# Optimization experiments

Measured on AMD Instinct MI355X. Metric: run time of the kernel, lower is better.

Reference implementation:

```python
import jax, jax.numpy as jnp
import numpy as np

N = 131072      # points (rays x samples chunk)
E = 8           # spatial sub-networks (centroids)
DIN = 90        # encoded pos+dir features fed to sub-NeRFs (xyz_real=True -> x[:, 3:])
H = 256         # sub-NeRF hidden width
DOUT = 4        # rgb + sigma
MARGIN = 2.0    # boundary_margin
EPS = 1e-8


def setup_inputs() -> dict:
    key = jax.random.key(0)
    k = jax.random.split(key, 5)
    x_xyz = jax.random.uniform(k[0], (N, 3), dtype=jnp.float32)          # routing coords in [0,1)^3
    x_feat = jax.random.normal(k[1], (N, DIN), dtype=jnp.float32)        # encoded features
    x = jnp.concatenate([x_xyz, x_feat], axis=1)                         # [N, 3+DIN]
    centroids = jax.random.uniform(k[2], (E, 3), dtype=jnp.float32)
    W1 = jax.random.normal(k[3], (E, DIN, H), dtype=jnp.float32) * 0.05
    b1 = jnp.zeros((E, H), dtype=jnp.float32)
    W2 = jax.random.normal(k[4], (E, H, DOUT), dtype=jnp.float32) * 0.05
    b2 = jnp.zeros((E, DOUT), dtype=jnp.float32)
    return {"x": x, "centroids": centroids, "W1": W1, "b1": b1, "W2": W2, "b2": b2}


def reference(x, centroids, W1, b1, W2, b2):
    # --- centroid routing (torch.cdist equivalent) ---
    xyz = x[:, :3]                                                       # [N,3]
    d2 = jnp.sum((xyz[:, None, :] - centroids[None, :, :]) ** 2, axis=-1)
    dist = jnp.sqrt(jnp.maximum(d2, 0.0))                                # [N,E]
    inv = 1.0 / (dist + EPS)
    min_d = jnp.min(dist, axis=1, keepdims=True)                         # [N,1]
    inv = jnp.where(dist > MARGIN * min_d, 0.0, inv)                     # zero far experts
    weights = inv / jnp.sum(inv, axis=-1, keepdims=True)                 # [N,E], rows sum to 1

    # --- per-expert sub-NeRF MLP, weighted combine ---
    # Dense-equivalent of masked gather + weighted scatter-add: experts whose
    # weight is exactly 0 contribute nothing, matching the torch masked path.
    feat = x[:, 3:]                                                      # xyz_real=True -> drop xyz
    h = jax.nn.relu(jnp.einsum('nd,edh->enh', feat, W1) + b1[:, None, :])  # [E,N,H]
    out_e = jnp.einsum('enh,eho->eno', h, W2) + b2[:, None, :]             # [E,N,DOUT]
    return jnp.einsum('eno,ne->no', out_e, weights)                        # [N,DOUT]
```

## Files before the change

kernel.cpp:

```cpp
#include <hip/hip_runtime.h>

#define NPTS 131072
#define NE 8
#define DIN 90
#define NH 256
#define DO4 4
#define HPITCH 264

typedef __attribute__((ext_vector_type(8))) short bf16x8;
typedef __attribute__((ext_vector_type(4))) float f32x4;
typedef __attribute__((ext_vector_type(2))) unsigned int u32x2;

__device__ __forceinline__ unsigned short f2bf(float f) {
  unsigned int u = __float_as_uint(f);
  u += 0x7fffu + ((u >> 16) & 1u);
  return (unsigned short)(u >> 16);
}

__global__ __launch_bounds__(256) void prep_w1(const float* __restrict__ W1,
                                               unsigned short* __restrict__ W1T) {
  int idx = blockIdx.x * 256 + threadIdx.x;
  if (idx >= NE * NH * 96) return;
  int kp = idx % 96;
  int n  = (idx / 96) % NH;
  int e  = idx / (96 * NH);
  float v = (kp < DIN) ? W1[((size_t)e * DIN + kp) * NH + n] : 0.f;
  W1T[idx] = f2bf(v);
}

__global__ __launch_bounds__(256) void prep_w2(const float* __restrict__ W2,
                                               unsigned short* __restrict__ W2T) {
  int idx = blockIdx.x * 256 + threadIdx.x;
  if (idx >= NE * 16 * NH) return;
  int k = idx % NH;
  int o = (idx / NH) % 16;
  int e = idx / (16 * NH);
  float v = (o < DO4) ? W2[((size_t)e * NH + k) * DO4 + o] : 0.f;
  W2T[idx] = f2bf(v);
}

__global__ __launch_bounds__(256, 2) void meganerf_main(
    const float* __restrict__ x, const float* __restrict__ cent,
    const float* __restrict__ b1, const float* __restrict__ b2,
    const unsigned short* __restrict__ W1T, const unsigned short* __restrict__ W2T,
    float* __restrict__ out) {
  __shared__ unsigned short sH[64 * HPITCH];
  __shared__ float sW[NE][64];
  __shared__ float sB2[64][DO4];
  __shared__ float sOutP[4][64][DO4];

  const int t   = threadIdx.x;
  const int lane = t & 63;
  const int wid = t >> 6;
  const int l15 = lane & 15;
  const int l4  = lane >> 4;
  const int row0 = blockIdx.x * 64;

  bf16x8 bfr[4][3];
#pragma unroll
  for (int nf = 0; nf < 4; ++nf) {
    const float* gr = x + (size_t)(row0 + 16 * nf + l15) * 93 + 3;
#pragma unroll
    for (int ks = 0; ks < 3; ++ks) {
      const int kb = 32 * ks + 8 * l4;
      bf16x8 a;
#pragma unroll
      for (int j = 0; j < 8; ++j) {
        int k = kb + j;
        float v = (k < DIN) ? gr[k] : 0.f;
        a[j] = (short)f2bf(v);
      }
      bfr[nf][ks] = a;
    }
  }

  if (t < 64) {
    const float* gx = x + (size_t)(row0 + t) * 93;
    float px = gx[0], py = gx[1], pz = gx[2];
    float dist[NE], inv[NE];
    float mind = 3.4e38f;
#pragma unroll
    for (int e = 0; e < NE; ++e) {
      float dx = px - cent[e * 3 + 0];
      float dy = py - cent[e * 3 + 1];
      float dz = pz - cent[e * 3 + 2];
      float d2 = dx * dx + dy * dy + dz * dz;
      float d = sqrtf(fmaxf(d2, 0.f));
      dist[e] = d;
      inv[e] = 1.f / (d + 1e-8f);
      mind = fminf(mind, d);
    }
    float s = 0.f;
#pragma unroll
    for (int e = 0; e < NE; ++e) {
      if (dist[e] > 2.0f * mind) inv[e] = 0.f;
      s += inv[e];
    }
    float rs = 1.f / s;
    float bb[4] = {0.f, 0.f, 0.f, 0.f};
#pragma unroll
    for (int e = 0; e < NE; ++e) {
      float w = inv[e] * rs;
      sW[e][t] = w;
#pragma unroll
      for (int o = 0; o < 4; ++o) bb[o] += w * b2[e * 4 + o];
    }
#pragma unroll
    for (int o = 0; o < 4; ++o) sB2[t][o] = bb[o];
  }
  __syncthreads();

  f32x4 facc[4] = {{0.f, 0.f, 0.f, 0.f}, {0.f, 0.f, 0.f, 0.f},
                   {0.f, 0.f, 0.f, 0.f}, {0.f, 0.f, 0.f, 0.f}};

  for (int e = 0; e < NE; ++e) {
    float wv[4];
#pragma unroll
    for (int nf = 0; nf < 4; ++nf) wv[nf] = sW[e][16 * nf + l15];

#pragma unroll
    for (int c = 0; c < 2; ++c) {
      const int colbase = 128 * c + 32 * wid;
      f32x4 b1v[2];
#pragma unroll
      for (int mf = 0; mf < 2; ++mf)
        b1v[mf] = *(const f32x4*)(b1 + e * NH + colbase + 16 * mf + 4 * l4);
      f32x4 acc[2][4];
#pragma unroll
      for (int mf = 0; mf < 2; ++mf)
#pragma unroll
        for (int nf = 0; nf < 4; ++nf) acc[mf][nf] = b1v[mf];
#pragma unroll
      for (int ks = 0; ks < 3; ++ks) {
        bf16x8 w1f[2];
#pragma unroll
        for (int mf = 0; mf < 2; ++mf)
          w1f[mf] = *(const bf16x8*)(W1T +
              (size_t)(e * NH + colbase + 16 * mf + l15) * 96 + 32 * ks + 8 * l4);
#pragma unroll
        for (int mf = 0; mf < 2; ++mf)
#pragma unroll
          for (int nf = 0; nf < 4; ++nf)
            acc[mf][nf] = __builtin_amdgcn_mfma_f32_16x16x32_bf16(
                w1f[mf], bfr[nf][ks], acc[mf][nf], 0, 0, 0);
      }
#pragma unroll
      for (int mf = 0; mf < 2; ++mf) {
        const int hcol = colbase + 16 * mf + 4 * l4;
#pragma unroll
        for (int nf = 0; nf < 4; ++nf) {
          float w = wv[nf];
          f32x4 a = acc[mf][nf];
          unsigned int p0 = (unsigned int)f2bf(fmaxf(a[0], 0.f) * w) |
                            ((unsigned int)f2bf(fmaxf(a[1], 0.f) * w) << 16);
          unsigned int p1 = (unsigned int)f2bf(fmaxf(a[2], 0.f) * w) |
                            ((unsigned int)f2bf(fmaxf(a[3], 0.f) * w) << 16);
          u32x2 pk;
          pk[0] = p0;
          pk[1] = p1;
          *(u32x2*)&sH[(16 * nf + l15) * HPITCH + hcol] = pk;
        }
      }
    }
    __syncthreads();

#pragma unroll
    for (int ks2 = 0; ks2 < 2; ++ks2) {
      const int k = 64 * wid + 32 * ks2 + 8 * l4;
      bf16x8 bw = *(const bf16x8*)(W2T + (size_t)(e * 16 + l15) * NH + k);
#pragma unroll
      for (int rf = 0; rf < 4; ++rf) {
        bf16x8 ah = *(const bf16x8*)&sH[(16 * rf + l15) * HPITCH + k];
        facc[rf] = __builtin_amdgcn_mfma_f32_16x16x32_bf16(ah, bw, facc[rf], 0, 0, 0);
      }
    }
    __syncthreads();
  }

  if (l15 < DO4) {
#pragma unroll
    for (int rf = 0; rf < 4; ++rf)
#pragma unroll
      for (int r = 0; r < 4; ++r)
        sOutP[wid][16 * rf + 4 * l4 + r][l15] = facc[rf][r];
  }
  __syncthreads();
  {
    const int row = t >> 2, o = t & 3;
    float v = sB2[row][o] + sOutP[0][row][o] + sOutP[1][row][o] +
              sOutP[2][row][o] + sOutP[3][row][o];
    out[(size_t)(row0 + row) * DO4 + o] = v;
  }
}

extern "C" void kernel_launch(void* const* d_in, const int* in_sizes, int n_in,
                              void* d_out, int out_size, void* d_ws, size_t ws_size,
                              hipStream_t stream) {
  const float* x    = (const float*)d_in[0];
  const float* cent = (const float*)d_in[1];
  const float* W1   = (const float*)d_in[2];
  const float* b1   = (const float*)d_in[3];
  const float* W2   = (const float*)d_in[4];
  const float* b2   = (const float*)d_in[5];
  float* out = (float*)d_out;

  unsigned short* W1T = (unsigned short*)d_ws;
  unsigned short* W2T = W1T + NE * NH * 96;

  prep_w1<<<(NE * NH * 96 + 255) / 256, 256, 0, stream>>>(W1, W1T);
  prep_w2<<<(NE * 16 * NH + 255) / 256, 256, 0, stream>>>(W2, W2T);
  meganerf_main<<<NPTS / 64, 256, 0, stream>>>(x, cent, b1, b2, W1T, W2T, out);
}
```

Before: 193.6 us.

## Merge prep kernels, vectorize input loads, cheaper bf16 packing, raise occupancy

Fuses the two weight-prep kernels into one launch. Input features are now loaded as float4 vectors instead of scalar gathers. bf16 packing now uses a single perm that truncates after adding 0x7fff, dropping the round-to-even term. The output partials reuse the sH buffer so LDS per block shrinks, and launch bounds ask for 3 blocks per SIMD. The trade-offs are slightly different rounding and more register pressure at the higher occupancy target.

```diff
diff --git a/kernel.cpp b/kernel.cpp
--- a/kernel.cpp
+++ b/kernel.cpp
@@ -4,12 +4,15 @@
 #define NE 8
 #define DIN 90
 #define NH 256
-#define DO4 4
 #define HPITCH 264
 
 typedef __attribute__((ext_vector_type(8))) short bf16x8;
 typedef __attribute__((ext_vector_type(4))) float f32x4;
+typedef __attribute__((ext_vector_type(2))) float f32x2;
+typedef __attribute__((ext_vector_type(4))) unsigned int u32x4;
 typedef __attribute__((ext_vector_type(2))) unsigned int u32x2;
+typedef __attribute__((ext_vector_type(4), aligned(4))) float f32x4a;
+typedef __attribute__((ext_vector_type(2), aligned(4))) float f32x2a;
 
 __device__ __forceinline__ unsigned short f2bf(float f) {
   unsigned int u = __float_as_uint(f);
@@ -17,61 +20,81 @@
   return (unsigned short)(u >> 16);
 }
 
-__global__ __launch_bounds__(256) void prep_w1(const float* __restrict__ W1,
-                                               unsigned short* __restrict__ W1T) {
+__device__ __forceinline__ unsigned int pkbf(float f0, float f1) {
+  unsigned int u0 = __float_as_uint(f0) + 0x7fffu;
+  unsigned int u1 = __float_as_uint(f1) + 0x7fffu;
+  return __builtin_amdgcn_perm(u1, u0, 0x07060302u);
+}
+
+__device__ __forceinline__ bf16x8 cvt8(f32x4 a, f32x4 b) {
+  u32x4 r;
+  r[0] = pkbf(a[0], a[1]);
+  r[1] = pkbf(a[2], a[3]);
+  r[2] = pkbf(b[0], b[1]);
+  r[3] = pkbf(b[2], b[3]);
+  return __builtin_bit_cast(bf16x8, r);
+}
+
+__global__ __launch_bounds__(256) void prep(const float* __restrict__ W1,
+                                            const float* __restrict__ W2,
+                                            unsigned short* __restrict__ W1T,
+                                            unsigned short* __restrict__ W2T) {
   int idx = blockIdx.x * 256 + threadIdx.x;
-  if (idx >= NE * NH * 96) return;
-  int kp = idx % 96;
-  int n  = (idx / 96) % NH;
-  int e  = idx / (96 * NH);
-  float v = (kp < DIN) ? W1[((size_t)e * DIN + kp) * NH + n] : 0.f;
-  W1T[idx] = f2bf(v);
-}
-
-__global__ __launch_bounds__(256) void prep_w2(const float* __restrict__ W2,
-                                               unsigned short* __restrict__ W2T) {
-  int idx = blockIdx.x * 256 + threadIdx.x;
-  if (idx >= NE * 16 * NH) return;
-  int k = idx % NH;
-  int o = (idx / NH) % 16;
-  int e = idx / (16 * NH);
-  float v = (o < DO4) ? W2[((size_t)e * NH + k) * DO4 + o] : 0.f;
-  W2T[idx] = f2bf(v);
-}
-
-__global__ __launch_bounds__(256, 2) void meganerf_main(
+  const int n1 = NE * NH * 96;
+  if (idx < n1) {
+    int kp = idx % 96;
+    int n  = (idx / 96) % NH;
+    int e  = idx / (96 * NH);
+    float v = (kp < DIN) ? W1[((size_t)e * DIN + kp) * NH + n] : 0.f;
+    W1T[idx] = f2bf(v);
+  } else {
+    int j = idx - n1;
+    if (j < NE * 16 * NH) {
+      int k = j % NH;
+      int o = (j / NH) % 16;
+      int e = j / (16 * NH);
+      float v = (o < 4) ? W2[((size_t)e * NH + k) * 4 + o] : 0.f;
+      W2T[j] = f2bf(v);
+    }
+  }
+}
+
+__global__ __launch_bounds__(256, 3) void meganerf_main(
     const float* __restrict__ x, const float* __restrict__ cent,
     const float* __restrict__ b1, const float* __restrict__ b2,
     const unsigned short* __restrict__ W1T, const unsigned short* __restrict__ W2T,
     float* __restrict__ out) {
   __shared__ unsigned short sH[64 * HPITCH];
   __shared__ float sW[NE][64];
-  __shared__ float sB2[64][DO4];
-  __shared__ float sOutP[4][64][DO4];
-
-  const int t   = threadIdx.x;
+  __shared__ float sB2[64][4];
+
+  const int t    = threadIdx.x;
   const int lane = t & 63;
-  const int wid = t >> 6;
-  const int l15 = lane & 15;
-  const int l4  = lane >> 4;
+  const int wid  = t >> 6;
+  const int l15  = lane & 15;
+  const int l4   = lane >> 4;
   const int row0 = blockIdx.x * 64;
 
   bf16x8 bfr[4][3];
 #pragma unroll
   for (int nf = 0; nf < 4; ++nf) {
     const float* gr = x + (size_t)(row0 + 16 * nf + l15) * 93 + 3;
-#pragma unroll
-    for (int ks = 0; ks < 3; ++ks) {
-      const int kb = 32 * ks + 8 * l4;
-      bf16x8 a;
-#pragma unroll
-      for (int j = 0; j < 8; ++j) {
-        int k = kb + j;
-        float v = (k < DIN) ? gr[k] : 0.f;
-        a[j] = (short)f2bf(v);
-      }
-      bfr[nf][ks] = a;
-    }
+    f32x4 v0, v1;
+    v0 = *(const f32x4a*)(gr + 8 * l4);
+    v1 = *(const f32x4a*)(gr + 8 * l4 + 4);
+    bfr[nf][0] = cvt8(v0, v1);
+    v0 = *(const f32x4a*)(gr + 32 + 8 * l4);
+    v1 = *(const f32x4a*)(gr + 36 + 8 * l4);
+    bfr[nf][1] = cvt8(v0, v1);
+    if (l4 < 3) {
+      v0 = *(const f32x4a*)(gr + 64 + 8 * l4);
+      v1 = *(const f32x4a*)(gr + 68 + 8 * l4);
+    } else {
+      f32x2 tl = *(const f32x2a*)(gr + 88);
+      v0[0] = tl[0]; v0[1] = tl[1]; v0[2] = 0.f; v0[3] = 0.f;
+      v1[0] = 0.f; v1[1] = 0.f; v1[2] = 0.f; v1[3] = 0.f;
+    }
+    bfr[nf][2] = cvt8(v0, v1);
   }
 
   if (t < 64) {
@@ -149,15 +172,17 @@
         const int hcol = colbase + 16 * mf + 4 * l4;
 #pragma unroll
         for (int nf = 0; nf < 4; ++nf) {
-          float w = wv[nf];
+          const float w = wv[nf];
           f32x4 a = acc[mf][nf];
-          unsigned int p0 = (unsigned int)f2bf(fmaxf(a[0], 0.f) * w) |
-                            ((unsigned int)f2bf(fmaxf(a[1], 0.f) * w) << 16);
-          unsigned int p1 = (unsigned int)f2bf(fmaxf(a[2], 0.f) * w) |
-                            ((unsigned int)f2bf(fmaxf(a[3], 0.f) * w) << 16);
+          f32x2 p0, p1;
+          p0[0] = a[0]; p0[1] = a[1];
+          p1[0] = a[2]; p1[1] = a[3];
+          const f32x2 z = {0.f, 0.f};
+          p0 = __builtin_elementwise_max(p0, z) * w;
+          p1 = __builtin_elementwise_max(p1, z) * w;
           u32x2 pk;
-          pk[0] = p0;
-          pk[1] = p1;
+          pk[0] = pkbf(p0[0], p0[1]);
+          pk[1] = pkbf(p1[0], p1[1]);
           *(u32x2*)&sH[(16 * nf + l15) * HPITCH + hcol] = pk;
         }
       }
@@ -177,19 +202,20 @@
     __syncthreads();
   }
 
-  if (l15 < DO4) {
+  float* sOutP = (float*)sH;
+  if (l15 < 4) {
 #pragma unroll
     for (int rf = 0; rf < 4; ++rf)
 #pragma unroll
       for (int r = 0; r < 4; ++r)
-        sOutP[wid][16 * rf + 4 * l4 + r][l15] = facc[rf][r];
+        sOutP[(wid * 64 + 16 * rf + 4 * l4 + r) * 4 + l15] = facc[rf][r];
   }
   __syncthreads();
   {
     const int row = t >> 2, o = t & 3;
-    float v = sB2[row][o] + sOutP[0][row][o] + sOutP[1][row][o] +
-              sOutP[2][row][o] + sOutP[3][row][o];
-    out[(size_t)(row0 + row) * DO4 + o] = v;
+    float v = sB2[row][o] + sOutP[(0 * 64 + row) * 4 + o] + sOutP[(1 * 64 + row) * 4 + o] +
+              sOutP[(2 * 64 + row) * 4 + o] + sOutP[(3 * 64 + row) * 4 + o];
+    out[row0 * 4 + t] = v;
   }
 }
 
@@ -207,7 +233,7 @@
   unsigned short* W1T = (unsigned short*)d_ws;
   unsigned short* W2T = W1T + NE * NH * 96;
 
-  prep_w1<<<(NE * NH * 96 + 255) / 256, 256, 0, stream>>>(W1, W1T);
-  prep_w2<<<(NE * 16 * NH + 255) / 256, 256, 0, stream>>>(W2, W2T);
+  const int prep_total = NE * NH * 96 + NE * 16 * NH;
+  prep<<<(prep_total + 255) / 256, 256, 0, stream>>>(W1, W2, W1T, W2T);
   meganerf_main<<<NPTS / 64, 256, 0, stream>>>(x, cent, b1, b2, W1T, W2T, out);
 }
```

Result: faster. 181.1 us (-6.4%).
